# Performance work log

Measured on AMD Instinct MI355X. Metric: run time of the kernel, lower is better.

## Reference

```python
import jax, jax.numpy as jnp
import numpy as np

N_NODES = 100000
FEAT = 256
HID = 128
REL = 2
BATCH = 20000
K = 10  # filtersize


def setup_inputs() -> dict:
    key = jax.random.key(0)
    k1, k2, k3, k4, k5 = jax.random.split(key, 5)
    nodes = jax.random.randint(k1, (BATCH,), 0, N_NODES)
    neigh_idx = jax.random.randint(k2, (REL, BATCH, K), 0, N_NODES)
    features = jax.random.normal(k3, (N_NODES, FEAT), dtype=jnp.float32)
    W_stc = jax.random.normal(k4, (REL, FEAT, HID), dtype=jnp.float32) * (1.0 / np.sqrt(FEAT))
    W_det = jax.random.normal(k5, (FEAT + REL * HID, HID), dtype=jnp.float32) * (1.0 / np.sqrt(FEAT + REL * HID))
    return {"nodes": nodes, "neigh_idx": neigh_idx, "features": features,
            "W_stc": W_stc, "W_det": W_det}


def reference(nodes, neigh_idx, features, W_stc, W_det):
    # self features: irregular gather [B, F]
    self_feats = features[nodes]
    # per-relation neighbor gather [R, B, K, F] -> mean over sampled neighbors [R, B, F]
    neigh_mean = features[neigh_idx].mean(axis=2)
    # STC layer projection to hidden per relation: [R, B, H]
    neigh_h = jnp.einsum('rbf,rfh->rbh', neigh_mean, W_stc)
    # concat self feats with each relation's neighbor embedding: [B, F + R*H]
    combined = jnp.concatenate(
        [self_feats, jnp.moveaxis(neigh_h, 0, 1).reshape(neigh_h.shape[1], -1)], axis=1)
    # linear + relu (dropout_flag=False -> no dropout)
    return jax.nn.relu(combined @ W_det)
```

## Files before the change

### kernel.cpp

```cpp
#include <hip/hip_runtime.h>
#include <hip/hip_bf16.h>

#define N_NODES 100000
#define FEAT    256
#define HID     128
#define REL     2
#define BATCH   20000
#define KNEI    10

#define APAD    8
#define AROW    (768 + APAD)

typedef short bf16x8 __attribute__((ext_vector_type(8)));
typedef float f32x4  __attribute__((ext_vector_type(4)));

__device__ __forceinline__ unsigned short f2bf(float x) {
    union { float f; unsigned u; } v; v.f = x;
    unsigned r = v.u + 0x7fffu + ((v.u >> 16) & 1u);
    return (unsigned short)(r >> 16);
}

__device__ __forceinline__ ushort4 pack4(float a, float b, float c, float d) {
    ushort4 p; p.x = f2bf(a); p.y = f2bf(b); p.z = f2bf(c); p.w = f2bf(d);
    return p;
}

__device__ __forceinline__ size_t bsw_index(int k, int n) {
    int kt = k >> 5, j = k & 7, hi = (k >> 3) & 3;
    int lane = hi * 16 + (n & 15), nt = n >> 4;
    return ((size_t)(kt * 8 + nt) * 64 + lane) * 8 + j;
}

__global__ __launch_bounds__(256) void prep_B(const float* __restrict__ W_stc,
                                              const float* __restrict__ W_det,
                                              unsigned short* __restrict__ Bsw) {
    const int blk = blockIdx.x;
    const int tid = threadIdx.x;
    if (blk < 32) {
        const int rel   = blk >> 4;
        const int fbase = (blk & 15) * 16;
        const int n     = tid & 127;
        const int fh    = tid >> 7;
        const float* wd = W_det + (size_t)(256 + rel * HID) * HID + n;
        #pragma unroll
        for (int fo = 0; fo < 8; ++fo) {
            const int f = fbase + fh * 8 + fo;
            const float* ws = W_stc + (size_t)(rel * FEAT + f) * HID;
            float acc = 0.f;
            #pragma unroll 8
            for (int j2 = 0; j2 < HID; ++j2) acc += ws[j2] * wd[(size_t)j2 * HID];
            const int k = 256 + rel * 256 + f;
            Bsw[bsw_index(k, n)] = f2bf(acc);
        }
    } else {
        const int base = (blk - 32) * 16384;
        #pragma unroll 4
        for (int i = 0; i < 64; ++i) {
            const int idx = base + i * 256 + tid;
            const int k = idx >> 7, n = idx & 127;
            Bsw[bsw_index(k, n)] = f2bf(W_det[idx]);
        }
    }
}

__global__ __launch_bounds__(256, 4) void fused(const int* __restrict__ nodes,
                                                const int* __restrict__ neigh_idx,
                                                const float* __restrict__ features,
                                                const unsigned short* __restrict__ Bsw,
                                                float* __restrict__ out) {
    __shared__ unsigned short As[16 * AROW];

    const int blk  = blockIdx.x;
    const int w    = threadIdx.x >> 6;
    const int lane = threadIdx.x & 63;
    const float4* F4 = (const float4*)features;
    const float inv = 1.0f / (float)KNEI;

    #pragma unroll
    for (int e = 0; e < 4; ++e) {
        const int m = w * 4 + e;
        const int b = blk * 16 + m;
        const int self = nodes[b];
        const int* i0 = neigh_idx + (size_t)b * KNEI;
        const int* i1 = neigh_idx + (size_t)(BATCH + b) * KNEI;

        float4 sf = F4[(size_t)self * 64 + lane];
        float4 s0 = make_float4(0.f, 0.f, 0.f, 0.f);
        float4 s1 = make_float4(0.f, 0.f, 0.f, 0.f);
        #pragma unroll
        for (int k = 0; k < KNEI; ++k) {
            float4 v = F4[(size_t)i0[k] * 64 + lane];
            s0.x += v.x; s0.y += v.y; s0.z += v.z; s0.w += v.w;
        }
        #pragma unroll
        for (int k = 0; k < KNEI; ++k) {
            float4 v = F4[(size_t)i1[k] * 64 + lane];
            s1.x += v.x; s1.y += v.y; s1.z += v.z; s1.w += v.w;
        }
        ushort4* row = (ushort4*)(As + m * AROW);
        row[lane]       = pack4(sf.x, sf.y, sf.z, sf.w);
        row[64 + lane]  = pack4(s0.x * inv, s0.y * inv, s0.z * inv, s0.w * inv);
        row[128 + lane] = pack4(s1.x * inv, s1.y * inv, s1.z * inv, s1.w * inv);
    }
    __syncthreads();

    const int quad = lane >> 4;
    const int l16  = lane & 15;
    const unsigned short* a_base = As + l16 * AROW + quad * 8;

    f32x4 acc0 = (f32x4){0.f, 0.f, 0.f, 0.f};
    f32x4 acc1 = (f32x4){0.f, 0.f, 0.f, 0.f};
    const int nt0 = w, nt1 = w + 4;

    #pragma unroll
    for (int kt = 0; kt < 24; ++kt) {
        bf16x8 a = *(const bf16x8*)(a_base + kt * 32);
        const unsigned short* bk = Bsw + ((size_t)(kt * 8) * 64 + lane) * 8;
        bf16x8 b0 = *(const bf16x8*)(bk + (size_t)nt0 * 64 * 8);
        bf16x8 b1 = *(const bf16x8*)(bk + (size_t)nt1 * 64 * 8);
        acc0 = __builtin_amdgcn_mfma_f32_16x16x32_bf16(a, b0, acc0, 0, 0, 0);
        acc1 = __builtin_amdgcn_mfma_f32_16x16x32_bf16(a, b1, acc1, 0, 0, 0);
    }

    float* orow = out + (size_t)(blk * 16) * HID;
    #pragma unroll
    for (int r = 0; r < 4; ++r) {
        const int row = quad * 4 + r;
        float v0 = acc0[r];
        float v1 = acc1[r];
        orow[(size_t)row * HID + nt0 * 16 + l16] = v0 > 0.f ? v0 : 0.f;
        orow[(size_t)row * HID + nt1 * 16 + l16] = v1 > 0.f ? v1 : 0.f;
    }
}

extern "C" void kernel_launch(void* const* d_in, const int* in_sizes, int n_in,
                              void* d_out, int out_size, void* d_ws, size_t ws_size,
                              hipStream_t stream) {
    const int*   nodes     = (const int*)d_in[0];
    const int*   neigh_idx = (const int*)d_in[1];
    const float* features  = (const float*)d_in[2];
    const float* W_stc     = (const float*)d_in[3];
    const float* W_det     = (const float*)d_in[4];
    float* out = (float*)d_out;

    unsigned short* Bsw = (unsigned short*)d_ws;

    prep_B<<<34, 256, 0, stream>>>(W_stc, W_det, Bsw);
    fused<<<BATCH / 16, 256, 0, stream>>>(nodes, neigh_idx, features, Bsw, out);
}
```

Before: 231.8 us.

## Parallelize weight prep across more blocks and batch gather loads with LDS indices

The weight-folding prep kernel goes from 34 blocks with serial per-thread loops to 272 blocks, each thread computing one output. This removes a long serial prologue that used only a few CUs. In the fused kernel, each block first stages all of its node and neighbor indices in shared memory with coalesced loads. Each thread then issues all 21 feature-row loads before accumulating, to raise memory-level parallelism. The cost is higher register pressure from 21 float4 temporaries, which may hurt occupancy under the launch bounds.

Result: faster. 197.4 us (-14.8%).

```diff
diff --git a/kernel.cpp b/kernel.cpp
--- a/kernel.cpp
+++ b/kernel.cpp
@@ -36,26 +36,20 @@
                                               unsigned short* __restrict__ Bsw) {
     const int blk = blockIdx.x;
     const int tid = threadIdx.x;
-    if (blk < 32) {
-        const int rel   = blk >> 4;
-        const int fbase = (blk & 15) * 16;
-        const int n     = tid & 127;
-        const int fh    = tid >> 7;
+    if (blk < 256) {
+        const int rel = blk >> 7;
+        const int f   = (blk & 127) * 2 + (tid >> 7);
+        const int n   = tid & 127;
+        const float* ws = W_stc + (size_t)(rel * FEAT + f) * HID;
         const float* wd = W_det + (size_t)(256 + rel * HID) * HID + n;
+        float acc = 0.f;
         #pragma unroll
-        for (int fo = 0; fo < 8; ++fo) {
-            const int f = fbase + fh * 8 + fo;
-            const float* ws = W_stc + (size_t)(rel * FEAT + f) * HID;
-            float acc = 0.f;
-            #pragma unroll 8
-            for (int j2 = 0; j2 < HID; ++j2) acc += ws[j2] * wd[(size_t)j2 * HID];
-            const int k = 256 + rel * 256 + f;
-            Bsw[bsw_index(k, n)] = f2bf(acc);
-        }
+        for (int j = 0; j < HID; ++j) acc += ws[j] * wd[(size_t)j * HID];
+        Bsw[bsw_index(256 + rel * 256 + f, n)] = f2bf(acc);
     } else {
-        const int base = (blk - 32) * 16384;
-        #pragma unroll 4
-        for (int i = 0; i < 64; ++i) {
+        const int base = (blk - 256) * 2048;
+        #pragma unroll
+        for (int i = 0; i < 8; ++i) {
             const int idx = base + i * 256 + tid;
             const int k = idx >> 7, n = idx & 127;
             Bsw[bsw_index(k, n)] = f2bf(W_det[idx]);
@@ -69,36 +63,55 @@
                                                 const unsigned short* __restrict__ Bsw,
                                                 float* __restrict__ out) {
     __shared__ unsigned short As[16 * AROW];
+    __shared__ int idxs[336];
 
     const int blk  = blockIdx.x;
-    const int w    = threadIdx.x >> 6;
-    const int lane = threadIdx.x & 63;
+    const int tid  = threadIdx.x;
+    const int w    = tid >> 6;
+    const int lane = tid & 63;
     const float4* F4 = (const float4*)features;
     const float inv = 1.0f / (float)KNEI;
+
+    {
+        if (tid < 16)       idxs[tid] = nodes[blk * 16 + tid];
+        else if (tid < 176) idxs[tid] = neigh_idx[blk * 160 + (tid - 16)];
+        else                idxs[tid] = neigh_idx[BATCH * KNEI + blk * 160 + (tid - 176)];
+        const int t2 = tid + 256;
+        if (t2 < 336)       idxs[t2] = neigh_idx[BATCH * KNEI + blk * 160 + (t2 - 176)];
+    }
+    __syncthreads();
 
     #pragma unroll
     for (int e = 0; e < 4; ++e) {
         const int m = w * 4 + e;
-        const int b = blk * 16 + m;
-        const int self = nodes[b];
-        const int* i0 = neigh_idx + (size_t)b * KNEI;
-        const int* i1 = neigh_idx + (size_t)(BATCH + b) * KNEI;
+        const int* i0 = &idxs[16 + m * KNEI];
+        const int* i1 = &idxs[176 + m * KNEI];
 
-        float4 sf = F4[(size_t)self * 64 + lane];
-        float4 s0 = make_float4(0.f, 0.f, 0.f, 0.f);
-        float4 s1 = make_float4(0.f, 0.f, 0.f, 0.f);
+        float4 ta[11];
+        ta[0] = F4[(size_t)idxs[m] * 64 + lane];
         #pragma unroll
-        for (int k = 0; k < KNEI; ++k) {
-            float4 v = F4[(size_t)i0[k] * 64 + lane];
-            s0.x += v.x; s0.y += v.y; s0.z += v.z; s0.w += v.w;
+        for (int k = 0; k < KNEI; ++k)
+            ta[1 + k] = F4[(size_t)i0[k] * 64 + lane];
+        float4 tb[10];
+        #pragma unroll
+        for (int k = 0; k < KNEI; ++k)
+            tb[k] = F4[(size_t)i1[k] * 64 + lane];
+
+        float4 s0 = ta[1];
+        #pragma unroll
+        for (int k = 1; k < KNEI; ++k) {
+            s0.x += ta[1 + k].x; s0.y += ta[1 + k].y;
+            s0.z += ta[1 + k].z; s0.w += ta[1 + k].w;
         }
+        float4 s1 = tb[0];
         #pragma unroll
-        for (int k = 0; k < KNEI; ++k) {
-            float4 v = F4[(size_t)i1[k] * 64 + lane];
-            s1.x += v.x; s1.y += v.y; s1.z += v.z; s1.w += v.w;
+        for (int k = 1; k < KNEI; ++k) {
+            s1.x += tb[k].x; s1.y += tb[k].y;
+            s1.z += tb[k].z; s1.w += tb[k].w;
         }
+
         ushort4* row = (ushort4*)(As + m * AROW);
-        row[lane]       = pack4(sf.x, sf.y, sf.z, sf.w);
+        row[lane]       = pack4(ta[0].x, ta[0].y, ta[0].z, ta[0].w);
         row[64 + lane]  = pack4(s0.x * inv, s0.y * inv, s0.z * inv, s0.w * inv);
         row[128 + lane] = pack4(s1.x * inv, s1.y * inv, s1.z * inv, s1.w * inv);
     }
@@ -145,6 +158,6 @@
 
     unsigned short* Bsw = (unsigned short*)d_ws;
 
-    prep_B<<<34, 256, 0, stream>>>(W_stc, W_det, Bsw);
+    prep_B<<<272, 256, 0, stream>>>(W_stc, W_det, Bsw);
     fused<<<BATCH / 16, 256, 0, stream>>>(nodes, neigh_idx, features, Bsw, out);
 }
```
